# Kernel tuning notes

Hardware: AMD Instinct MI355X
Metric: run time of the kernel (lower is better)

Reference implementation:

```python
import jax, jax.numpy as jnp
import numpy as np


def _gcn_norm(edge_index, num_nodes):
    # PyG GCNConv default: add self-loops, symmetric normalization.
    src, dst = edge_index[0], edge_index[1]
    loop = jnp.arange(num_nodes, dtype=edge_index.dtype)
    src = jnp.concatenate([src, loop])
    dst = jnp.concatenate([dst, loop])
    deg = jax.ops.segment_sum(jnp.ones_like(dst, dtype=jnp.float32), dst,
                              num_segments=num_nodes)
    dinv = jnp.where(deg > 0, jax.lax.rsqrt(deg), 0.0)
    norm = dinv[src] * dinv[dst]  # [E + N]
    return src, dst, norm


def _gcn_conv(x, src, dst, norm, W, b):
    h = x @ W                      # [N, F_out]
    msg = h[src] * norm[:, None]   # gather + scale, [E+N, F_out]
    agg = jax.ops.segment_sum(msg, dst, num_segments=x.shape[0])
    return agg + b


def reference(x, edge_index, W1, b1, W2, b2, Wfc, bfc):
    N = x.shape[0]
    src, dst, norm = _gcn_norm(edge_index, N)
    h = jax.nn.relu(_gcn_conv(x, src, dst, norm, W1, b1))
    h = jax.nn.relu(_gcn_conv(h, src, dst, norm, W2, b2))
    return h @ Wfc + bfc  # [N, 2]


def setup_inputs() -> dict:
    N, E, D, OUT = 50000, 800000, 128, 2
    key = jax.random.key(0)
    ks = jax.random.split(key, 6)
    s = 1.0 / np.sqrt(D)
    return {
        "x": jax.random.normal(ks[0], (N, D), dtype=jnp.float32),
        "edge_index": jax.random.randint(ks[1], (2, E), 0, N, dtype=jnp.int32),
        "W1": jax.random.normal(ks[2], (D, D), dtype=jnp.float32) * s,
        "b1": jnp.zeros((D,), dtype=jnp.float32),
        "W2": jax.random.normal(ks[3], (D, D), dtype=jnp.float32) * s,
        "b2": jnp.zeros((D,), dtype=jnp.float32),
        "Wfc": jax.random.normal(ks[4], (D, OUT), dtype=jnp.float32) * s,
        "bfc": jnp.zeros((OUT,), dtype=jnp.float32),
    }
```

## Files before the change

### kernel.cpp

```cpp
#include <hip/hip_runtime.h>
#include <hip/hip_fp16.h>

#define D 128
#define GEMM_TM 64
#define EDGE_BLOCKS 4096
#define CAP 64

typedef _Float16 f16x8 __attribute__((ext_vector_type(8)));
typedef float f32x4 __attribute__((ext_vector_type(4)));

__global__ void k_zero(int4* __restrict__ p, int n4) {
    int i = blockIdx.x * 256 + threadIdx.x;
    if (i < n4) p[i] = make_int4(0, 0, 0, 0);
}

__global__ void k_dinv(const int* __restrict__ fill, float* __restrict__ dinv, int N) {
    int i = blockIdx.x * 256 + threadIdx.x;
    if (i < N) dinv[i] = rsqrtf((float)(fill[i] + 1));
}

__device__ __forceinline__ void stage_wt(const float* __restrict__ W, f16x8* wt) {
#pragma unroll
    for (int i = 0; i < 8; ++i) {
        int u = i * 256 + threadIdx.x;
        int c = u & 127;
        int k0 = (u >> 7) * 8;
        f16x8 v;
#pragma unroll
        for (int j = 0; j < 8; ++j) v[j] = (_Float16)W[(k0 + j) * D + c];
        wt[u] = v;
    }
}

__device__ __forceinline__ void mfma_rows(const f16x8 af[4], const f16x8* wt,
                                          __half* __restrict__ Y,
                                          int row_base, int N, int lane,
                                          const float sc[4]) {
    int kg = lane >> 4;
    int c15 = lane & 15;
#pragma unroll
    for (int ct = 0; ct < 8; ++ct) {
        f32x4 acc = {0.f, 0.f, 0.f, 0.f};
#pragma unroll
        for (int ks = 0; ks < 4; ++ks) {
            f16x8 bf = wt[(ks * 4 + kg) * 128 + ct * 16 + c15];
            acc = __builtin_amdgcn_mfma_f32_16x16x32_f16(af[ks], bf, acc, 0, 0, 0);
        }
        int c = ct * 16 + c15;
#pragma unroll
        for (int r = 0; r < 4; ++r) {
            int grow = row_base + kg * 4 + r;
            if (grow < N) Y[(size_t)grow * D + c] = __float2half(sc[r] * acc[r]);
        }
    }
}

__global__ __launch_bounds__(256) void k_gemm1_bin(const float* __restrict__ X,
                                                   const float* __restrict__ W1,
                                                   __half* __restrict__ T1,
                                                   int NV,
                                                   const int* __restrict__ src,
                                                   const int* __restrict__ dst,
                                                   int* __restrict__ fill,
                                                   unsigned short* __restrict__ col,
                                                   int E) {
    __shared__ f16x8 wt[2048];
    int b = blockIdx.x;
    if (b < EDGE_BLOCKS) {
        int r = b & 7;
        int lo = (r * NV) >> 3;
        int hi = ((r + 1) * NV) >> 3;
        int idx = (b >> 3) * 256 + threadIdx.x;
        const int stride4 = (EDGE_BLOCKS / 8) * 256 * 4;
        int4 dv[2], sv[2];
        bool hv[2];
#pragma unroll
        for (int k = 0; k < 2; ++k) {
            int e4 = idx * 4 + k * stride4;
            hv[k] = (e4 + 4 <= E);
            if (hv[k]) {
                dv[k] = *(const int4*)(dst + e4);
                sv[k] = *(const int4*)(src + e4);
            }
        }
#pragma unroll
        for (int k = 0; k < 2; ++k) {
            if (hv[k]) {
#pragma unroll
                for (int j = 0; j < 4; ++j) {
                    int d = (j == 0) ? dv[k].x : (j == 1) ? dv[k].y : (j == 2) ? dv[k].z : dv[k].w;
                    int s = (j == 0) ? sv[k].x : (j == 1) ? sv[k].y : (j == 2) ? sv[k].z : sv[k].w;
                    if (d >= lo && d < hi) {
                        int pos = atomicAdd(&fill[d], 1);
                        if (pos < CAP) col[(size_t)d * CAP + pos] = (unsigned short)s;
                    }
                }
            } else {
                for (int e = idx * 4 + k * stride4; e < E; ++e) {
                    int d = dst[e];
                    if (d >= lo && d < hi) {
                        int s = src[e];
                        int pos = atomicAdd(&fill[d], 1);
                        if (pos < CAP) col[(size_t)d * CAP + pos] = (unsigned short)s;
                    }
                }
            }
        }
        return;
    }
    int gb = b - EDGE_BLOCKS;
    stage_wt(W1, wt);
    __syncthreads();

    int lane = threadIdx.x & 63, w = threadIdx.x >> 6;
    int tile_row = gb * GEMM_TM + w * 16;
    int ar = tile_row + (lane & 15);
    const float* xr = X + (size_t)(ar < NV ? ar : NV - 1) * D;
    int kg = lane >> 4;
    f16x8 af[4];
#pragma unroll
    for (int ks = 0; ks < 4; ++ks) {
        float4 lo4 = *(const float4*)(xr + ks * 32 + kg * 8);
        float4 hi4 = *(const float4*)(xr + ks * 32 + kg * 8 + 4);
        f16x8 v = {(_Float16)lo4.x, (_Float16)lo4.y, (_Float16)lo4.z, (_Float16)lo4.w,
                   (_Float16)hi4.x, (_Float16)hi4.y, (_Float16)hi4.z, (_Float16)hi4.w};
        af[ks] = v;
    }
    const float one4[4] = {1.f, 1.f, 1.f, 1.f};
    mfma_rows(af, wt, T1, tile_row, NV, lane, one4);
}

__global__ __launch_bounds__(256) void k_gemm2(const __half* __restrict__ H,
                                               const float* __restrict__ W2,
                                               const float* __restrict__ dinv,
                                               __half* __restrict__ T2, int N) {
    __shared__ f16x8 wt[2048];
    stage_wt(W2, wt);
    __syncthreads();

    int lane = threadIdx.x & 63, w = threadIdx.x >> 6;
    int tile_row = blockIdx.x * GEMM_TM + w * 16;
    int ar = tile_row + (lane & 15);
    const __half* hr = H + (size_t)(ar < N ? ar : N - 1) * D;
    int kg = lane >> 4;
    f16x8 af[4];
#pragma unroll
    for (int ks = 0; ks < 4; ++ks)
        af[ks] = *(const f16x8*)(hr + ks * 32 + kg * 8);
    float sc[4];
#pragma unroll
    for (int r = 0; r < 4; ++r) {
        int grow = tile_row + kg * 4 + r;
        sc[r] = (grow < N) ? dinv[grow] : 1.f;
    }
    mfma_rows(af, wt, T2, tile_row, N, lane, sc);
}

template <int MODE>
__device__ __forceinline__ void agg_core(const __half* __restrict__ T,
                                         const float* __restrict__ dinv,
                                         const unsigned short* __restrict__ col,
                                         int n, int lane, int deg,
                                         float acc[8]) {
    int l4 = lane & 15;
    int g = lane >> 4;
#pragma unroll
    for (int j = 0; j < 8; ++j) acc[j] = 0.f;
    int base = n * CAP;
    int dcap = deg < CAP ? deg : CAP;
    int last = base + dcap - 1;

    for (int it = 0; it < dcap; it += 8) {
        int ei0 = it + g;
        int ei1 = it + 4 + g;
        bool a0 = ei0 < dcap, a1 = ei1 < dcap;
        int e0 = a0 ? base + ei0 : last;
        int e1 = a1 ? base + ei1 : last;
        int s0 = (int)col[e0];
        int s1 = (int)col[e1];
        float w0, w1;
        if (MODE == 0) {
            w0 = a0 ? dinv[s0] : 0.f;
            w1 = a1 ? dinv[s1] : 0.f;
        } else {
            w0 = a0 ? 1.f : 0.f;
            w1 = a1 ? 1.f : 0.f;
        }
        f16x8 v0 = *(const f16x8*)(T + (size_t)s0 * D + l4 * 8);
        f16x8 v1 = *(const f16x8*)(T + (size_t)s1 * D + l4 * 8);
#pragma unroll
        for (int j = 0; j < 8; ++j) {
            acc[j] = fmaf(w0, (float)v0[j], acc[j]);
            acc[j] = fmaf(w1, (float)v1[j], acc[j]);
        }
    }
#pragma unroll
    for (int j = 0; j < 8; ++j) {
        acc[j] += __shfl_down(acc[j], 32);
        acc[j] += __shfl_down(acc[j], 16);
    }
}

__global__ __launch_bounds__(256) void agg_relu(const __half* __restrict__ T,
                                                const int* __restrict__ fill,
                                                const float* __restrict__ dinv,
                                                const unsigned short* __restrict__ col,
                                                const float* __restrict__ bias,
                                                __half* __restrict__ H, int N) {
    int n = (blockIdx.x * blockDim.x + threadIdx.x) >> 6;
    int lane = threadIdx.x & 63;
    if (n >= N) return;
    n = __builtin_amdgcn_readfirstlane(n);
    int deg = fill[n];
    float dn = dinv[n];
    float acc[8];
    agg_core<0>(T, dinv, col, n, lane, deg, acc);
    if (lane < 16) {
        int l4 = lane;
        f16x8 self = *(const f16x8*)(T + (size_t)n * D + l4 * 8);
        f32x4 b0 = *(const f32x4*)(bias + l4 * 8);
        f32x4 b1 = *(const f32x4*)(bias + l4 * 8 + 4);
        f16x8 o;
#pragma unroll
        for (int j = 0; j < 8; ++j) {
            float t = acc[j] + dn * (float)self[j];
            float bj = (j < 4) ? b0[j] : b1[j - 4];
            o[j] = (_Float16)fmaxf(fmaf(dn, t, bj), 0.f);
        }
        *(f16x8*)(H + (size_t)n * D + l4 * 8) = o;
    }
}

__global__ __launch_bounds__(256) void agg_fc(const __half* __restrict__ T,
                                              const int* __restrict__ fill,
                                              const float* __restrict__ dinv,
                                              const unsigned short* __restrict__ col,
                                              const float* __restrict__ b2,
                                              const float* __restrict__ Wfc,
                                              const float* __restrict__ bfc,
                                              float* __restrict__ out, int N) {
    int n = (blockIdx.x * blockDim.x + threadIdx.x) >> 6;
    int lane = threadIdx.x & 63;
    if (n >= N) return;
    n = __builtin_amdgcn_readfirstlane(n);
    int deg = fill[n];
    float dn = dinv[n];
    float acc[8];
    agg_core<1>(T, dinv, col, n, lane, deg, acc);
    int l4 = lane & 15;
    f16x8 self = *(const f16x8*)(T + (size_t)n * D + l4 * 8);
    f32x4 b0 = *(const f32x4*)(b2 + l4 * 8);
    f32x4 b1 = *(const f32x4*)(b2 + l4 * 8 + 4);
    float o0 = 0.f, o1 = 0.f;
#pragma unroll
    for (int j = 0; j < 8; ++j) {
        float t = acc[j] + (float)self[j];
        float bj = (j < 4) ? b0[j] : b1[j - 4];
        float h = fmaxf(fmaf(dn, t, bj), 0.f);
        float2 wf = ((const float2*)Wfc)[l4 * 8 + j];
        o0 = fmaf(h, wf.x, o0);
        o1 = fmaf(h, wf.y, o1);
    }
#pragma unroll
    for (int off = 8; off > 0; off >>= 1) {
        o0 += __shfl_xor(o0, off);
        o1 += __shfl_xor(o1, off);
    }
    if (lane == 0) {
        out[(size_t)n * 2 + 0] = o0 + bfc[0];
        out[(size_t)n * 2 + 1] = o1 + bfc[1];
    }
}


extern "C" void kernel_launch(void* const* d_in, const int* in_sizes, int n_in,
                              void* d_out, int out_size, void* d_ws, size_t ws_size,
                              hipStream_t stream) {
    const float* x   = (const float*)d_in[0];
    const int* ei    = (const int*)d_in[1];
    const float* W1  = (const float*)d_in[2];
    const float* b1  = (const float*)d_in[3];
    const float* W2  = (const float*)d_in[4];
    const float* b2  = (const float*)d_in[5];
    const float* Wfc = (const float*)d_in[6];
    const float* bfc = (const float*)d_in[7];
    float* out = (float*)d_out;

    const int N = in_sizes[0] / D;
    const int E = in_sizes[1] / 2;
    const int* src = ei;
    const int* dst = ei + E;

    __half* t1  = (__half*)d_ws;
    __half* h16 = t1 + (size_t)N * D;
    __half* t2  = h16 + (size_t)N * D;
    int* fill   = (int*)(t2 + (size_t)N * D);
    float* dinv = (float*)(fill + N);
    unsigned short* col = (unsigned short*)(dinv + N);

    int n4 = (N + 3) / 4;
    k_zero<<<(n4 + 255) / 256, 256, 0, stream>>>((int4*)fill, n4);

    int gblocks = (int)((N + GEMM_TM - 1) / GEMM_TM);
    int nblocks = (N + 255) / 256;

    k_gemm1_bin<<<EDGE_BLOCKS + gblocks, 256, 0, stream>>>(
        x, W1, t1, N, src, dst, fill, col, E);

    k_dinv<<<nblocks, 256, 0, stream>>>(fill, dinv, N);

    int ablocks = (N + 3) / 4;
    agg_relu<<<ablocks, 256, 0, stream>>>(t1, fill, dinv, col, b1, h16, N);

    k_gemm2<<<gblocks, 256, 0, stream>>>(h16, W2, dinv, t2, N);

    agg_fc<<<ablocks, 256, 0, stream>>>(t2, fill, dinv, col, b2, Wfc, bfc, out, N);
}
```

Before: 139.1 us.

## Pad neighbor lists to 16 with a zero sentinel row and unroll aggregation

Each node's neighbor list is padded up to a multiple of 16 using a sentinel index N, which points at an added zero row in T1/T2 and has dinv[N]=0. This lets the aggregation loop drop its predication and issue four gathers per iteration instead of two. Edge binning now runs as a grid-stride loop over half as many blocks, and GEMM loads and stores use nontemporal hints. The cost is extra padding work in k_dinv, shifted workspace offsets, and some wasted gathers for low-degree nodes.

```diff
diff --git a/kernel.cpp b/kernel.cpp
--- a/kernel.cpp
+++ b/kernel.cpp
@@ -3,20 +3,36 @@
 
 #define D 128
 #define GEMM_TM 64
-#define EDGE_BLOCKS 4096
+#define EDGE_BLOCKS 2048
 #define CAP 64
 
 typedef _Float16 f16x8 __attribute__((ext_vector_type(8)));
 typedef float f32x4 __attribute__((ext_vector_type(4)));
+typedef int i32x4 __attribute__((ext_vector_type(4)));
 
 __global__ void k_zero(int4* __restrict__ p, int n4) {
     int i = blockIdx.x * 256 + threadIdx.x;
     if (i < n4) p[i] = make_int4(0, 0, 0, 0);
 }
 
-__global__ void k_dinv(const int* __restrict__ fill, float* __restrict__ dinv, int N) {
+__global__ void k_dinv(const int* __restrict__ fill, float* __restrict__ dinv,
+                       unsigned short* __restrict__ col,
+                       __half* __restrict__ t1, __half* __restrict__ t2, int N) {
     int i = blockIdx.x * 256 + threadIdx.x;
-    if (i < N) dinv[i] = rsqrtf((float)(fill[i] + 1));
+    if (i < N) {
+        int deg = fill[i];
+        if (deg > CAP) deg = CAP;
+        dinv[i] = rsqrtf((float)(deg + 1));
+        int dpad = (deg + 15) & ~15;
+        for (int p = deg; p < dpad; ++p)
+            col[(size_t)i * CAP + p] = (unsigned short)N;
+    } else if (i == N) {
+        dinv[N] = 0.f;
+    }
+    if (i < D) {
+        t1[(size_t)N * D + i] = __ushort_as_half((unsigned short)0);
+        t2[(size_t)N * D + i] = __ushort_as_half((unsigned short)0);
+    }
 }
 
 __device__ __forceinline__ void stage_wt(const float* __restrict__ W, f16x8* wt) {
@@ -50,7 +66,10 @@
 #pragma unroll
         for (int r = 0; r < 4; ++r) {
             int grow = row_base + kg * 4 + r;
-            if (grow < N) Y[(size_t)grow * D + c] = __float2half(sc[r] * acc[r]);
+            if (grow < N) {
+                unsigned short hv = __half_as_ushort(__float2half(sc[r] * acc[r]));
+                __builtin_nontemporal_store(hv, (unsigned short*)&Y[(size_t)grow * D + c]);
+            }
         }
     }
 }
@@ -71,32 +90,22 @@
         int lo = (r * NV) >> 3;
         int hi = ((r + 1) * NV) >> 3;
         int idx = (b >> 3) * 256 + threadIdx.x;
-        const int stride4 = (EDGE_BLOCKS / 8) * 256 * 4;
-        int4 dv[2], sv[2];
-        bool hv[2];
-#pragma unroll
-        for (int k = 0; k < 2; ++k) {
-            int e4 = idx * 4 + k * stride4;
-            hv[k] = (e4 + 4 <= E);
-            if (hv[k]) {
-                dv[k] = *(const int4*)(dst + e4);
-                sv[k] = *(const int4*)(src + e4);
-            }
-        }
-#pragma unroll
-        for (int k = 0; k < 2; ++k) {
-            if (hv[k]) {
+        int stride4 = (EDGE_BLOCKS / 8) * 256 * 4;
+        for (int e4 = idx * 4; e4 < E; e4 += stride4) {
+            if (e4 + 4 <= E) {
+                i32x4 dv = __builtin_nontemporal_load((const i32x4*)(dst + e4));
+                i32x4 sv = __builtin_nontemporal_load((const i32x4*)(src + e4));
 #pragma unroll
                 for (int j = 0; j < 4; ++j) {
-                    int d = (j == 0) ? dv[k].x : (j == 1) ? dv[k].y : (j == 2) ? dv[k].z : dv[k].w;
-                    int s = (j == 0) ? sv[k].x : (j == 1) ? sv[k].y : (j == 2) ? sv[k].z : sv[k].w;
+                    int d = dv[j];
+                    int s = sv[j];
                     if (d >= lo && d < hi) {
                         int pos = atomicAdd(&fill[d], 1);
                         if (pos < CAP) col[(size_t)d * CAP + pos] = (unsigned short)s;
                     }
                 }
             } else {
-                for (int e = idx * 4 + k * stride4; e < E; ++e) {
+                for (int e = e4; e < E; ++e) {
                     int d = dst[e];
                     if (d >= lo && d < hi) {
                         int s = src[e];
@@ -120,10 +129,10 @@
     f16x8 af[4];
 #pragma unroll
     for (int ks = 0; ks < 4; ++ks) {
-        float4 lo4 = *(const float4*)(xr + ks * 32 + kg * 8);
-        float4 hi4 = *(const float4*)(xr + ks * 32 + kg * 8 + 4);
-        f16x8 v = {(_Float16)lo4.x, (_Float16)lo4.y, (_Float16)lo4.z, (_Float16)lo4.w,
-                   (_Float16)hi4.x, (_Float16)hi4.y, (_Float16)hi4.z, (_Float16)hi4.w};
+        f32x4 lo4 = __builtin_nontemporal_load((const f32x4*)(xr + ks * 32 + kg * 8));
+        f32x4 hi4 = __builtin_nontemporal_load((const f32x4*)(xr + ks * 32 + kg * 8 + 4));
+        f16x8 v = {(_Float16)lo4[0], (_Float16)lo4[1], (_Float16)lo4[2], (_Float16)lo4[3],
+                   (_Float16)hi4[0], (_Float16)hi4[1], (_Float16)hi4[2], (_Float16)hi4[3]};
         af[ks] = v;
     }
     const float one4[4] = {1.f, 1.f, 1.f, 1.f};
@@ -146,7 +155,7 @@
     f16x8 af[4];
 #pragma unroll
     for (int ks = 0; ks < 4; ++ks)
-        af[ks] = *(const f16x8*)(hr + ks * 32 + kg * 8);
+        af[ks] = __builtin_nontemporal_load((const f16x8*)(hr + ks * 32 + kg * 8));
     float sc[4];
 #pragma unroll
     for (int r = 0; r < 4; ++r) {
@@ -168,30 +177,30 @@
     for (int j = 0; j < 8; ++j) acc[j] = 0.f;
     int base = n * CAP;
     int dcap = deg < CAP ? deg : CAP;
-    int last = base + dcap - 1;
-
-    for (int it = 0; it < dcap; it += 8) {
-        int ei0 = it + g;
-        int ei1 = it + 4 + g;
-        bool a0 = ei0 < dcap, a1 = ei1 < dcap;
-        int e0 = a0 ? base + ei0 : last;
-        int e1 = a1 ? base + ei1 : last;
-        int s0 = (int)col[e0];
-        int s1 = (int)col[e1];
-        float w0, w1;
+    int dpad = (dcap + 15) & ~15;
+
+    for (int it = 0; it < dpad; it += 16) {
+        int e = base + it + g;
+        int s0 = (int)col[e];
+        int s1 = (int)col[e + 4];
+        int s2 = (int)col[e + 8];
+        int s3 = (int)col[e + 12];
+        float w0, w1, w2, w3;
         if (MODE == 0) {
-            w0 = a0 ? dinv[s0] : 0.f;
-            w1 = a1 ? dinv[s1] : 0.f;
+            w0 = dinv[s0]; w1 = dinv[s1]; w2 = dinv[s2]; w3 = dinv[s3];
         } else {
-            w0 = a0 ? 1.f : 0.f;
-            w1 = a1 ? 1.f : 0.f;
+            w0 = w1 = w2 = w3 = 1.f;
         }
         f16x8 v0 = *(const f16x8*)(T + (size_t)s0 * D + l4 * 8);
         f16x8 v1 = *(const f16x8*)(T + (size_t)s1 * D + l4 * 8);
+        f16x8 v2 = *(const f16x8*)(T + (size_t)s2 * D + l4 * 8);
+        f16x8 v3 = *(const f16x8*)(T + (size_t)s3 * D + l4 * 8);
 #pragma unroll
         for (int j = 0; j < 8; ++j) {
             acc[j] = fmaf(w0, (float)v0[j], acc[j]);
             acc[j] = fmaf(w1, (float)v1[j], acc[j]);
+            acc[j] = fmaf(w2, (float)v2[j], acc[j]);
+            acc[j] = fmaf(w3, (float)v3[j], acc[j]);
         }
     }
 #pragma unroll
@@ -292,22 +301,22 @@
     const int* dst = ei + E;
 
     __half* t1  = (__half*)d_ws;
-    __half* h16 = t1 + (size_t)N * D;
+    __half* h16 = t1 + (size_t)(N + 1) * D;
     __half* t2  = h16 + (size_t)N * D;
-    int* fill   = (int*)(t2 + (size_t)N * D);
+    int* fill   = (int*)(t2 + (size_t)(N + 1) * D);
     float* dinv = (float*)(fill + N);
-    unsigned short* col = (unsigned short*)(dinv + N);
+    unsigned short* col = (unsigned short*)(dinv + N + 1);
 
     int n4 = (N + 3) / 4;
     k_zero<<<(n4 + 255) / 256, 256, 0, stream>>>((int4*)fill, n4);
 
     int gblocks = (int)((N + GEMM_TM - 1) / GEMM_TM);
-    int nblocks = (N + 255) / 256;
 
     k_gemm1_bin<<<EDGE_BLOCKS + gblocks, 256, 0, stream>>>(
         x, W1, t1, N, src, dst, fill, col, E);
 
-    k_dinv<<<nblocks, 256, 0, stream>>>(fill, dinv, N);
+    int nb1 = (N + 1 + 255) / 256;
+    k_dinv<<<nb1, 256, 0, stream>>>(fill, dinv, col, t1, t2, N);
 
     int ablocks = (N + 3) / 4;
     agg_relu<<<ablocks, 256, 0, stream>>>(t1, fill, dinv, col, b1, h16, N);
```

Result: no change. 139.7 us (+0.5%).
